# Optimization experiments

Hardware: AMD Instinct MI355X
Metric: run time of the kernel (lower is better)

## Reference

```python
import jax, jax.numpy as jnp
import numpy as np


def setup_inputs() -> dict:
    key = jax.random.key(0)
    k1, k2 = jax.random.split(key)
    N, M, D = 16384, 16384, 3
    x = jax.random.normal(k1, (N, D), dtype=jnp.float32)
    y = jax.random.normal(k2, (M, D), dtype=jnp.float32)
    return {"x": x, "y": y}


def reference(x, y):
    # Squared euclidean pairwise distance matrix [N, M] (= torch.cdist(x, y).square()).
    x2 = jnp.sum(x * x, axis=-1, keepdims=True)          # [N, 1]
    y2 = jnp.sum(y * y, axis=-1, keepdims=True).T        # [1, M]
    dist = jnp.maximum(x2 + y2 - 2.0 * (x @ y.T), 0.0)   # [N, M]
    dist1 = jnp.min(dist, axis=1)                        # [N] nearest y for each x
    dist2 = jnp.min(dist, axis=0)                        # [M] nearest x for each y
    # reduction='mean'
    return (dist1.sum() + dist2.sum()) / (dist1.size + dist2.size)
```

## Files before the change

### kernel.cpp

```cpp
#include <hip/hip_runtime.h>


#define TPB 256
#define T 8
#define SLICES 128
#define LQ 128

__global__ void cd_prep(const float* __restrict__ x, const float* __restrict__ y,
                        float4* __restrict__ xp, float4* __restrict__ yp,
                        unsigned int* __restrict__ minx, unsigned int* __restrict__ miny,
                        int n, int mm) {
    int i = blockIdx.x * blockDim.x + threadIdx.x;
    const float* src = (i < n) ? x : y;
    int k = (i < n) ? i : i - n;
    if (i < n + mm) {
        float a = src[3 * k + 0];
        float b = src[3 * k + 1];
        float c = src[3 * k + 2];
        float4 v = make_float4(a, b, c, 0.5f * (a * a + b * b + c * c));
        if (i < n) { xp[k] = v; minx[k] = 0x7f800000u; }
        else       { yp[k] = v; miny[k] = 0x7f800000u; }
    }
}

__global__ __launch_bounds__(TPB) void cd_pass_dual(const float4* __restrict__ xp,
                                                    const float4* __restrict__ yp,
                                                    unsigned int* __restrict__ minx,
                                                    unsigned int* __restrict__ miny) {
    const float4* P;
    const float4* Q;
    unsigned int* out;
    if (blockIdx.z == 0) { P = xp; Q = yp; out = minx; }
    else                 { P = yp; Q = xp; out = miny; }

    __shared__ float4 qs[LQ];
    const int j0 = blockIdx.y * LQ;
    for (int j = threadIdx.x; j < LQ; j += TPB) qs[j] = Q[j0 + j];
    __syncthreads();

    const int base = blockIdx.x * (TPB * T) + threadIdx.x;
    float4 p[T];
    float m[T];
#pragma unroll
    for (int k = 0; k < T; ++k) {
        p[k] = P[base + k * TPB];
        m[k] = -INFINITY;
    }

#pragma unroll 16
    for (int j = 0; j < LQ; ++j) {
        float4 q = qs[j];
#pragma unroll
        for (int k = 0; k < T; ++k) {
            float acc = fmaf(p[k].x, q.x, -q.w);
            acc = fmaf(p[k].y, q.y, acc);
            acc = fmaf(p[k].z, q.z, acc);
            m[k] = fmaxf(m[k], acc);
        }
    }

#pragma unroll
    for (int k = 0; k < T; ++k) {
        float d = fmaxf(0.0f, 2.0f * (p[k].w - m[k]));
        atomicMin(&out[base + k * TPB], __float_as_uint(d));
    }
}

__global__ __launch_bounds__(1024) void cd_reduce(const uint4* __restrict__ minx,
                                                  const uint4* __restrict__ miny,
                                                  float* __restrict__ out, int n, int mm) {
    float s = 0.0f;
    for (int i = threadIdx.x; i < n / 4; i += 1024) {
        uint4 v = minx[i];
        s += __uint_as_float(v.x) + __uint_as_float(v.y) +
             __uint_as_float(v.z) + __uint_as_float(v.w);
    }
    for (int i = threadIdx.x; i < mm / 4; i += 1024) {
        uint4 v = miny[i];
        s += __uint_as_float(v.x) + __uint_as_float(v.y) +
             __uint_as_float(v.z) + __uint_as_float(v.w);
    }
    for (int off = 32; off >= 1; off >>= 1) s += __shfl_down(s, off, 64);
    __shared__ float wsum[16];
    int wave = threadIdx.x >> 6;
    int lane = threadIdx.x & 63;
    if (lane == 0) wsum[wave] = s;
    __syncthreads();
    if (threadIdx.x == 0) {
        float t = 0.0f;
        for (int w = 0; w < 16; ++w) t += wsum[w];
        out[0] = t / (float)(n + mm);
    }
}

extern "C" void kernel_launch(void* const* d_in, const int* in_sizes, int n_in,
                              void* d_out, int out_size, void* d_ws, size_t ws_size,
                              hipStream_t stream) {
    const float* x = (const float*)d_in[0];
    const float* y = (const float*)d_in[1];
    const int N = in_sizes[0] / 3;
    const int M = in_sizes[1] / 3;

    float4* xp = (float4*)d_ws;
    float4* yp = xp + N;
    unsigned int* minx = (unsigned int*)(yp + M);
    unsigned int* miny = minx + N;
    float* out = (float*)d_out;

    cd_prep<<<(N + M + TPB - 1) / TPB, TPB, 0, stream>>>(x, y, xp, yp, minx, miny, N, M);

    cd_pass_dual<<<dim3(N / (TPB * T), SLICES, 2), TPB, 0, stream>>>(xp, yp, minx, miny);

    cd_reduce<<<1, 1024, 0, stream>>>((const uint4*)minx, (const uint4*)miny, out, N, M);
}
```

Baseline: 52.69 us.

## Compute pairwise dot products with bf16 MFMA using split-precision encoding

Replaces the scalar FMA distance loop with 16x16x32 bf16 MFMA instructions. Each coordinate and the negated half-norm are split into three bf16 terms, and the products are laid out over 32 K-slots so the matrix core yields an fp32-accurate q·p - |q|^2/2. This is meant to move the O(N*M) arithmetic from vector ALUs onto matrix cores, at the cost of larger operand arrays, extra rounding terms and per-tile max reductions. The hardcoded NPTS also ties the grid to 16384 points.

```diff
diff --git a/kernel.cpp b/kernel.cpp
--- a/kernel.cpp
+++ b/kernel.cpp
@@ -1,68 +1,133 @@
 #include <hip/hip_runtime.h>
 
 
-#define TPB 256
-#define T 8
-#define SLICES 128
-#define LQ 128
+typedef short bf16x8 __attribute__((ext_vector_type(8)));
+typedef float f32x4 __attribute__((ext_vector_type(4)));
 
-__global__ void cd_prep(const float* __restrict__ x, const float* __restrict__ y,
-                        float4* __restrict__ xp, float4* __restrict__ yp,
-                        unsigned int* __restrict__ minx, unsigned int* __restrict__ miny,
-                        int n, int mm) {
-    int i = blockIdx.x * blockDim.x + threadIdx.x;
+#define NPTS   16384
+#define TPB    256
+#define OT     16
+#define SLICES 32
+#define QSL    (NPTS / SLICES)
+#define OPW    (OT * 16)
+#define OWAVES (NPTS / OPW)
+#define WPB    4
+
+__device__ __forceinline__ unsigned short f2b(float f) {
+    union { float f; unsigned u; } a; a.f = f;
+    return (unsigned short)((a.u + 0x7FFFu + ((a.u >> 16) & 1u)) >> 16);
+}
+__device__ __forceinline__ float b2f(unsigned short b) {
+    union { unsigned u; float f; } a; a.u = ((unsigned)b) << 16;
+    return a.f;
+}
+
+__global__ __launch_bounds__(TPB) void cd_prep(
+        const float* __restrict__ x, const float* __restrict__ y,
+        unsigned short* __restrict__ xA, unsigned short* __restrict__ xB,
+        unsigned short* __restrict__ yA, unsigned short* __restrict__ yB,
+        float* __restrict__ xh, float* __restrict__ yh,
+        unsigned* __restrict__ minx, unsigned* __restrict__ miny, int n, int m) {
+    int i = blockIdx.x * TPB + threadIdx.x;
+    if (i >= n + m) return;
     const float* src = (i < n) ? x : y;
     int k = (i < n) ? i : i - n;
-    if (i < n + mm) {
-        float a = src[3 * k + 0];
-        float b = src[3 * k + 1];
-        float c = src[3 * k + 2];
-        float4 v = make_float4(a, b, c, 0.5f * (a * a + b * b + c * c));
-        if (i < n) { xp[k] = v; minx[k] = 0x7f800000u; }
-        else       { yp[k] = v; miny[k] = 0x7f800000u; }
+    unsigned short* A = (i < n) ? xA : yA;
+    unsigned short* B = (i < n) ? xB : yB;
+    float* h = (i < n) ? xh : yh;
+    unsigned* mn = (i < n) ? minx : miny;
+
+    float v[3] = { src[3 * k], src[3 * k + 1], src[3 * k + 2] };
+    unsigned short sp[3][3];
+#pragma unroll
+    for (int d = 0; d < 3; ++d) {
+        float r = v[d];
+        sp[d][0] = f2b(r); r -= b2f(sp[d][0]);
+        sp[d][1] = f2b(r); r -= b2f(sp[d][1]);
+        sp[d][2] = f2b(r);
     }
+    float half = 0.5f * (v[0] * v[0] + v[1] * v[1] + v[2] * v[2]);
+    unsigned short ss[3];
+    { float r = -half;
+      ss[0] = f2b(r); r -= b2f(ss[0]);
+      ss[1] = f2b(r); r -= b2f(ss[1]);
+      ss[2] = f2b(r); }
+
+    unsigned short Av[32], Bv[32];
+#pragma unroll
+    for (int j = 0; j < 32; ++j) { Av[j] = 0; Bv[j] = 0; }
+#pragma unroll
+    for (int d = 0; d < 3; ++d)
+#pragma unroll
+        for (int a = 0; a < 3; ++a)
+#pragma unroll
+            for (int t = 0; t < 3; ++t) {
+                Av[d * 9 + a * 3 + t] = sp[d][t];
+                Bv[d * 9 + a * 3 + t] = sp[d][a];
+            }
+#pragma unroll
+    for (int a = 0; a < 3; ++a) { Av[27 + a] = ss[a]; Bv[27 + a] = 0x3F80; }
+
+    unsigned* Ao = (unsigned*)(A + (size_t)k * 32);
+    unsigned* Bo = (unsigned*)(B + (size_t)k * 32);
+#pragma unroll
+    for (int j = 0; j < 16; ++j) {
+        Ao[j] = (unsigned)Av[2 * j] | ((unsigned)Av[2 * j + 1] << 16);
+        Bo[j] = (unsigned)Bv[2 * j] | ((unsigned)Bv[2 * j + 1] << 16);
+    }
+    h[k] = half;
+    mn[k] = 0x7f800000u;
 }
 
-__global__ __launch_bounds__(TPB) void cd_pass_dual(const float4* __restrict__ xp,
-                                                    const float4* __restrict__ yp,
-                                                    unsigned int* __restrict__ minx,
-                                                    unsigned int* __restrict__ miny) {
-    const float4* P;
-    const float4* Q;
-    unsigned int* out;
-    if (blockIdx.z == 0) { P = xp; Q = yp; out = minx; }
-    else                 { P = yp; Q = xp; out = miny; }
+__global__ __launch_bounds__(TPB, 4) void cd_pass(
+        const unsigned short* __restrict__ xA, const unsigned short* __restrict__ xB,
+        const unsigned short* __restrict__ yA, const unsigned short* __restrict__ yB,
+        const float* __restrict__ xh, const float* __restrict__ yh,
+        unsigned* __restrict__ minx, unsigned* __restrict__ miny) {
+    const int lane = threadIdx.x & 63;
+    const int wave = threadIdx.x >> 6;
+    const int r = lane & 15, g = lane >> 4;
 
-    __shared__ float4 qs[LQ];
-    const int j0 = blockIdx.y * LQ;
-    for (int j = threadIdx.x; j < LQ; j += TPB) qs[j] = Q[j0 + j];
-    __syncthreads();
+    const unsigned short* Aq; const unsigned short* Bp;
+    const float* hs; unsigned* out;
+    if (blockIdx.z == 0) { Aq = yA; Bp = xB; hs = xh; out = minx; }
+    else                 { Aq = xA; Bp = yB; hs = yh; out = miny; }
 
-    const int base = blockIdx.x * (TPB * T) + threadIdx.x;
-    float4 p[T];
-    float m[T];
+    const int ow = blockIdx.x * WPB + wave;
+    const int obase = ow * OPW;
+
+    bf16x8 b[OT];
 #pragma unroll
-    for (int k = 0; k < T; ++k) {
-        p[k] = P[base + k * TPB];
-        m[k] = -INFINITY;
-    }
+    for (int o = 0; o < OT; ++o)
+        b[o] = *(const bf16x8*)(Bp + (size_t)(obase + o * 16 + r) * 32 + g * 8);
 
-#pragma unroll 16
-    for (int j = 0; j < LQ; ++j) {
-        float4 q = qs[j];
+    float mx[OT];
 #pragma unroll
-        for (int k = 0; k < T; ++k) {
-            float acc = fmaf(p[k].x, q.x, -q.w);
-            acc = fmaf(p[k].y, q.y, acc);
-            acc = fmaf(p[k].z, q.z, acc);
-            m[k] = fmaxf(m[k], acc);
+    for (int o = 0; o < OT; ++o) mx[o] = -INFINITY;
+
+    const int q0 = blockIdx.y * QSL;
+    const f32x4 zero = {0.f, 0.f, 0.f, 0.f};
+#pragma unroll 2
+    for (int t = 0; t < QSL / 16; ++t) {
+        bf16x8 a = *(const bf16x8*)(Aq + (size_t)(q0 + t * 16 + r) * 32 + g * 8);
+#pragma unroll
+        for (int o = 0; o < OT; ++o) {
+            f32x4 d = __builtin_amdgcn_mfma_f32_16x16x32_bf16(a, b[o], zero, 0, 0, 0);
+            mx[o] = fmaxf(mx[o], fmaxf(d[0], d[1]));
+            mx[o] = fmaxf(mx[o], fmaxf(d[2], d[3]));
         }
     }
 
 #pragma unroll
-    for (int k = 0; k < T; ++k) {
-        float d = fmaxf(0.0f, 2.0f * (p[k].w - m[k]));
-        atomicMin(&out[base + k * TPB], __float_as_uint(d));
+    for (int o = 0; o < OT; ++o) {
+        float vv = mx[o];
+        vv = fmaxf(vv, __shfl_xor(vv, 16, 64));
+        vv = fmaxf(vv, __shfl_xor(vv, 32, 64));
+        if (lane < 16) {
+            int id = obase + o * 16 + lane;
+            float dmin = fmaxf(0.0f, 2.0f * (hs[id] - vv));
+            atomicMin(&out[id], __float_as_uint(dmin));
+        }
     }
 }
 
@@ -101,15 +166,21 @@
     const int N = in_sizes[0] / 3;
     const int M = in_sizes[1] / 3;
 
-    float4* xp = (float4*)d_ws;
-    float4* yp = xp + N;
-    unsigned int* minx = (unsigned int*)(yp + M);
-    unsigned int* miny = minx + N;
+    unsigned short* xA = (unsigned short*)d_ws;
+    unsigned short* xB = xA + (size_t)N * 32;
+    unsigned short* yA = xB + (size_t)N * 32;
+    unsigned short* yB = yA + (size_t)M * 32;
+    float* xh = (float*)(yB + (size_t)M * 32);
+    float* yh = xh + N;
+    unsigned* minx = (unsigned*)(yh + M);
+    unsigned* miny = minx + N;
     float* out = (float*)d_out;
 
-    cd_prep<<<(N + M + TPB - 1) / TPB, TPB, 0, stream>>>(x, y, xp, yp, minx, miny, N, M);
+    cd_prep<<<(N + M + TPB - 1) / TPB, TPB, 0, stream>>>(x, y, xA, xB, yA, yB,
+                                                         xh, yh, minx, miny, N, M);
 
-    cd_pass_dual<<<dim3(N / (TPB * T), SLICES, 2), TPB, 0, stream>>>(xp, yp, minx, miny);
+    cd_pass<<<dim3(OWAVES / WPB, SLICES, 2), TPB, 0, stream>>>(xA, xB, yA, yB,
+                                                               xh, yh, minx, miny);
 
     cd_reduce<<<1, 1024, 0, stream>>>((const uint4*)minx, (const uint4*)miny, out, N, M);
 }
```

After: 66.79 us. 26.8% more time.

## Use packed FP32 FMA over paired query points with interleaved layout

Applied to the files above, without the earlier changes.

The prep kernel now also writes query points in a pair-interleaved layout (x0,x1,y0,y1,z0,z1,-h0,-h1). The inner loop loads two query points at once and evaluates both with v_pk_fma_f32 inline assembly, halving the FMA instruction count per pair. A max over the two lanes then follows. This adds extra workspace and prep writes, and hardcodes NPTS=16384 for the grid.

```diff
diff --git a/kernel.cpp b/kernel.cpp
--- a/kernel.cpp
+++ b/kernel.cpp
@@ -1,67 +1,88 @@
 #include <hip/hip_runtime.h>
 
 
-#define TPB 256
-#define T 8
+typedef float f32x2 __attribute__((ext_vector_type(2)));
+
+#define NPTS   16384
+#define TPB    256
+#define T      8
 #define SLICES 128
-#define LQ 128
+#define LQ     (NPTS / SLICES)
+#define PAIRS  (LQ / 2)
 
-__global__ void cd_prep(const float* __restrict__ x, const float* __restrict__ y,
-                        float4* __restrict__ xp, float4* __restrict__ yp,
-                        unsigned int* __restrict__ minx, unsigned int* __restrict__ miny,
-                        int n, int mm) {
-    int i = blockIdx.x * blockDim.x + threadIdx.x;
+__global__ __launch_bounds__(TPB) void cd_prep(
+        const float* __restrict__ x, const float* __restrict__ y,
+        float4* __restrict__ xp, float4* __restrict__ yp,
+        float* __restrict__ xq, float* __restrict__ yq,
+        unsigned* __restrict__ minx, unsigned* __restrict__ miny, int n, int m) {
+    int i = blockIdx.x * TPB + threadIdx.x;
+    if (i >= n + m) return;
     const float* src = (i < n) ? x : y;
     int k = (i < n) ? i : i - n;
-    if (i < n + mm) {
-        float a = src[3 * k + 0];
-        float b = src[3 * k + 1];
-        float c = src[3 * k + 2];
-        float4 v = make_float4(a, b, c, 0.5f * (a * a + b * b + c * c));
-        if (i < n) { xp[k] = v; minx[k] = 0x7f800000u; }
-        else       { yp[k] = v; miny[k] = 0x7f800000u; }
-    }
+    float a = src[3 * k], b = src[3 * k + 1], c = src[3 * k + 2];
+    float half = 0.5f * (a * a + b * b + c * c);
+    float4* pp = (i < n) ? xp : yp;
+    float* qq = (i < n) ? xq : yq;
+    unsigned* mn = (i < n) ? minx : miny;
+    pp[k] = make_float4(a, b, c, half);
+    int base = (k >> 1) * 8 + (k & 1);
+    qq[base + 0] = a;
+    qq[base + 2] = b;
+    qq[base + 4] = c;
+    qq[base + 6] = -half;
+    mn[k] = 0x7f800000u;
 }
 
-__global__ __launch_bounds__(TPB) void cd_pass_dual(const float4* __restrict__ xp,
-                                                    const float4* __restrict__ yp,
-                                                    unsigned int* __restrict__ minx,
-                                                    unsigned int* __restrict__ miny) {
-    const float4* P;
-    const float4* Q;
-    unsigned int* out;
-    if (blockIdx.z == 0) { P = xp; Q = yp; out = minx; }
-    else                 { P = yp; Q = xp; out = miny; }
+__global__ __launch_bounds__(TPB) void cd_pass(
+        const float4* __restrict__ xp, const float4* __restrict__ yp,
+        const float* __restrict__ xq, const float* __restrict__ yq,
+        unsigned* __restrict__ minx, unsigned* __restrict__ miny) {
+    const float4* P; const float* Q; unsigned* out;
+    if (blockIdx.z == 0) { P = xp; Q = yq; out = minx; }
+    else                 { P = yp; Q = xq; out = miny; }
 
-    __shared__ float4 qs[LQ];
+    __shared__ __align__(16) float qs[LQ * 4];
     const int j0 = blockIdx.y * LQ;
-    for (int j = threadIdx.x; j < LQ; j += TPB) qs[j] = Q[j0 + j];
+    const float4* srcq = (const float4*)(Q + (size_t)j0 * 4);
+    if (threadIdx.x < PAIRS * 2) ((float4*)qs)[threadIdx.x] = srcq[threadIdx.x];
     __syncthreads();
 
     const int base = blockIdx.x * (TPB * T) + threadIdx.x;
-    float4 p[T];
-    float m[T];
+    f32x2 px[T], py[T], pz[T];
+    float ph[T], m[T];
 #pragma unroll
     for (int k = 0; k < T; ++k) {
-        p[k] = P[base + k * TPB];
+        float4 p = P[base + k * TPB];
+        px[k] = (f32x2){p.x, p.x};
+        py[k] = (f32x2){p.y, p.y};
+        pz[k] = (f32x2){p.z, p.z};
+        ph[k] = p.w;
         m[k] = -INFINITY;
     }
 
-#pragma unroll 16
-    for (int j = 0; j < LQ; ++j) {
-        float4 q = qs[j];
+#pragma unroll 4
+    for (int jp = 0; jp < PAIRS; ++jp) {
+        f32x2 qx2 = *(const f32x2*)(qs + jp * 8 + 0);
+        f32x2 qy2 = *(const f32x2*)(qs + jp * 8 + 2);
+        f32x2 qz2 = *(const f32x2*)(qs + jp * 8 + 4);
+        f32x2 qw2 = *(const f32x2*)(qs + jp * 8 + 6);
 #pragma unroll
         for (int k = 0; k < T; ++k) {
-            float acc = fmaf(p[k].x, q.x, -q.w);
-            acc = fmaf(p[k].y, q.y, acc);
-            acc = fmaf(p[k].z, q.z, acc);
-            m[k] = fmaxf(m[k], acc);
+            f32x2 acc;
+            asm("v_pk_fma_f32 %0, %1, %2, %3\n\t"
+                "v_pk_fma_f32 %0, %4, %5, %0\n\t"
+                "v_pk_fma_f32 %0, %6, %7, %0"
+                : "=&v"(acc)
+                : "v"(px[k]), "v"(qx2), "v"(qw2),
+                  "v"(py[k]), "v"(qy2),
+                  "v"(pz[k]), "v"(qz2));
+            m[k] = fmaxf(m[k], fmaxf(acc.x, acc.y));
         }
     }
 
 #pragma unroll
     for (int k = 0; k < T; ++k) {
-        float d = fmaxf(0.0f, 2.0f * (p[k].w - m[k]));
+        float d = fmaxf(0.0f, 2.0f * (ph[k] - m[k]));
         atomicMin(&out[base + k * TPB], __float_as_uint(d));
     }
 }
@@ -103,13 +124,17 @@
 
     float4* xp = (float4*)d_ws;
     float4* yp = xp + N;
-    unsigned int* minx = (unsigned int*)(yp + M);
-    unsigned int* miny = minx + N;
+    float* xq = (float*)(yp + M);
+    float* yq = xq + (size_t)N * 4;
+    unsigned* minx = (unsigned*)(yq + (size_t)M * 4);
+    unsigned* miny = minx + N;
     float* out = (float*)d_out;
 
-    cd_prep<<<(N + M + TPB - 1) / TPB, TPB, 0, stream>>>(x, y, xp, yp, minx, miny, N, M);
+    cd_prep<<<(N + M + TPB - 1) / TPB, TPB, 0, stream>>>(x, y, xp, yp, xq, yq,
+                                                         minx, miny, N, M);
 
-    cd_pass_dual<<<dim3(N / (TPB * T), SLICES, 2), TPB, 0, stream>>>(xp, yp, minx, miny);
+    cd_pass<<<dim3(NPTS / (TPB * T), SLICES, 2), TPB, 0, stream>>>(xp, yp, xq, yq,
+                                                                   minx, miny);
 
     cd_reduce<<<1, 1024, 0, stream>>>((const uint4*)minx, (const uint4*)miny, out, N, M);
 }
```

Result: slower. 66.26 us (+25.8%).
